# Kernel optimization log

Hardware: AMD Instinct MI355X
Metric: run time of the kernel (lower is better)

The kernel has to match this reference:

```python
import jax, jax.numpy as jnp
import numpy as np

ITERS = 3

def squash(s, axis):
    # v = (|s|^2 / (1 + |s|^2)) * s / |s|
    sn = jnp.sum(s * s, axis=axis, keepdims=True)
    return sn / (1.0 + sn) * s / jnp.sqrt(sn)

def setup_inputs() -> dict:
    key = jax.random.key(0)
    k1, k2 = jax.random.split(key)
    b, B, C, P2, f = 8, 144, 16, 16, 12
    u = jax.random.normal(k1, (b, B, C, P2, f, f), dtype=jnp.float32)
    a = jax.random.uniform(k2, (b, B, f, f), dtype=jnp.float32)
    return {"u": u, "a": a}

def reference(u, a):
    # u: (b, B, C, P2, f, f); a: (b, B, f, f)
    b, B, C, P2, f, _ = u.shape
    # r: (b, B, C, 1, f, f), initialized uniform over C scaled by activation
    r = jnp.broadcast_to(a[:, :, None, None, :, :] * (1.0 / C), (b, B, C, 1, f, f))
    v = None
    for i in range(ITERS):
        c = jax.nn.softmax(r, axis=2)                       # over C
        v = squash(jnp.sum(c * u, axis=1, keepdims=True), axis=3)  # (b,1,C,P2,f,f)
        if i != ITERS - 1:
            r = r + jnp.sum(u * v, axis=3, keepdims=True)   # agreement over psize
    a_out = jnp.sqrt(jnp.sum(v * v, axis=3, keepdims=True))  # (b,1,C,1,f,f)
    return (jnp.squeeze(v, axis=1), jnp.squeeze(a_out, axis=(1, 3)))
```

## Files before the change

### kernel.cpp

```cpp
#include <hip/hip_runtime.h>
#include <math.h>


#define NB 8
#define BDIM 144
#define CDIM 16
#define PDIM 16
#define SDIM 144
#define PT 16
#define BC 8
#define NPT (SDIM / PT)
#define NBC (BDIM / BC)
#define USTRIDE (CDIM * PDIM * SDIM)
#define VELEMS (NB * CDIM * PDIM * SDIM)
#define NGROUP (NB * NPT)

__global__ __launch_bounds__(256) void route_kernel(
    const float* __restrict__ u, const float* __restrict__ a,
    float* __restrict__ V, float* __restrict__ s,
    unsigned int* __restrict__ cnt,
    float* __restrict__ out_v, float* __restrict__ out_a, int iter) {
  __shared__ float Vt[CDIM][PDIM][PT + 1];
  __shared__ float ebuf[2][CDIM][PT + 1];
  __shared__ float atile[BC][PT];
  __shared__ int isLast;

  const int tid = threadIdx.x;
  const int pos = tid & 15;
  const int c = tid >> 4;
  const int chunk = blockIdx.x;
  const int y = blockIdx.y;
  const int b = blockIdx.z;
  const int posg = y * PT + pos;
  const int B0 = chunk * BC;

  const float* ubase =
      u + ((size_t)((b * BDIM + B0) * CDIM + c) * PDIM) * SDIM + posg;

  float sacc[PDIM];
#pragma unroll
  for (int p = 0; p < PDIM; ++p) sacc[p] = 0.f;

  if (iter == 0) {
#pragma unroll 2
    for (int j = 0; j < BC; ++j) {
      const float* ub = ubase + (size_t)j * USTRIDE;
#pragma unroll
      for (int p = 0; p < PDIM; ++p) sacc[p] += ub[p * SDIM];
    }
#pragma unroll
    for (int p = 0; p < PDIM; ++p) sacc[p] *= (1.0f / CDIM);
  } else {
    float uvbuf[2][PDIM];
#pragma unroll
    for (int p = 0; p < PDIM; ++p) uvbuf[0][p] = ubase[p * SDIM];

    {
      const int vb = ((b * CDIM + c) * PDIM) * SDIM + posg;
#pragma unroll
      for (int p = 0; p < PDIM; ++p) Vt[c][p][pos] = V[vb + p * SDIM];
      if (tid < BC * PT) {
        const int j = tid >> 4;
        atile[j][pos] =
            a[(b * BDIM + B0 + j) * SDIM + y * PT + pos] * (1.0f / CDIM);
      }
    }
    __syncthreads();

#pragma unroll
    for (int j = 0; j < BC; ++j) {
      float* uv = uvbuf[j & 1];
      float* uvn = uvbuf[(j + 1) & 1];
      if (j + 1 < BC) {
        const float* ub = ubase + (size_t)(j + 1) * USTRIDE;
#pragma unroll
        for (int p = 0; p < PDIM; ++p) uvn[p] = ub[p * SDIM];
      }
      float dot = 0.f;
#pragma unroll
      for (int p = 0; p < PDIM; ++p) dot += uv[p] * Vt[c][p][pos];
      const float e = __expf(atile[j][pos] + dot);
      ebuf[j & 1][c][pos] = e;
      asm volatile("s_waitcnt lgkmcnt(0)" ::: "memory");
      __builtin_amdgcn_s_barrier();
      float sum = 0.f;
#pragma unroll
      for (int c2 = 0; c2 < CDIM; ++c2) sum += ebuf[j & 1][c2][pos];
      const float w = e * __builtin_amdgcn_rcpf(sum);
#pragma unroll
      for (int p = 0; p < PDIM; ++p) sacc[p] += w * uv[p];
    }
  }

  const int base = ((b * CDIM + c) * PDIM) * SDIM + posg;
#pragma unroll
  for (int p = 0; p < PDIM; ++p) atomicAdd(&s[base + p * SDIM], sacc[p]);

  asm volatile("s_waitcnt vmcnt(0)" ::: "memory");
  __syncthreads();
  if (tid == 0) {
    const unsigned old = atomicAdd(&cnt[b * NPT + y], 1u);
    isLast = (old == (NBC - 1));
  }
  __syncthreads();
  if (!isLast) return;

  float sv[PDIM];
  float sn = 0.f;
#pragma unroll
  for (int p = 0; p < PDIM; ++p) {
    const float x = s[base + p * SDIM];
    sv[p] = x;
    sn += x * x;
  }
  const float scale = sn / (1.0f + sn) * rsqrtf(sn);

  if (iter == 0) {
#pragma unroll
    for (int p = 0; p < PDIM; ++p) V[base + p * SDIM] = sv[p] * scale;
  } else if (iter == 1) {
#pragma unroll
    for (int p = 0; p < PDIM; ++p) V[base + p * SDIM] += sv[p] * scale;
  } else {
    float vv = 0.f;
#pragma unroll
    for (int p = 0; p < PDIM; ++p) {
      const float v = sv[p] * scale;
      out_v[base + p * SDIM] = v;
      vv += v * v;
    }
    out_a[(b * CDIM + c) * SDIM + posg] = sqrtf(vv);
  }
}


extern "C" void kernel_launch(void* const* d_in, const int* in_sizes, int n_in,
                              void* d_out, int out_size, void* d_ws, size_t ws_size,
                              hipStream_t stream) {
  const float* u = (const float*)d_in[0];
  const float* a = (const float*)d_in[1];
  float* out_v = (float*)d_out;
  float* out_a = out_v + VELEMS;

  float* V = (float*)d_ws;
  float* s = V + VELEMS;
  unsigned int* cnt = (unsigned int*)(s + (size_t)3 * VELEMS);

  hipMemsetAsync(s, 0, (size_t)3 * VELEMS * sizeof(float) +
                           3 * NGROUP * sizeof(unsigned int), stream);

  const dim3 g(NBC, NPT, NB);
  for (int it = 0; it < 3; ++it)
    route_kernel<<<g, 256, 0, stream>>>(u, a, V, s + (size_t)it * VELEMS,
                                        cnt + it * NGROUP, out_v, out_a, it);
}
```

Baseline: 358.8 us.

## Replace atomics and LDS softmax with float4 wave-shuffle kernels plus separate reduce

Restructures routing into a per-chunk kernel of 64-thread blocks, where each lane handles one capsule and four spatial positions via float4 loads. The softmax over capsules uses wave shuffles instead of shared memory and barriers. Partial sums are written to a per-chunk buffer rather than accumulated with atomics, and a second kernel reduces them and applies squash. This removes atomics, the last-block counter and the memset, but adds six kernel launches and extra partial-buffer traffic, and the blocks are small enough that occupancy may suffer.

```diff
diff --git a/kernel.cpp b/kernel.cpp
--- a/kernel.cpp
+++ b/kernel.cpp
@@ -7,129 +7,160 @@
 #define CDIM 16
 #define PDIM 16
 #define SDIM 144
+#define NF4 (SDIM / 4)
 #define PT 16
 #define BC 8
 #define NPT (SDIM / PT)
 #define NBC (BDIM / BC)
-#define USTRIDE (CDIM * PDIM * SDIM)
+#define UF4STRIDE ((size_t)CDIM * PDIM * NF4)
 #define VELEMS (NB * CDIM * PDIM * SDIM)
-#define NGROUP (NB * NPT)
+#define VF4 (VELEMS / 4)
 
-__global__ __launch_bounds__(256) void route_kernel(
+static __device__ __forceinline__ float4 f4zero() {
+  return make_float4(0.f, 0.f, 0.f, 0.f);
+}
+static __device__ __forceinline__ float4 f4add(float4 a, float4 b) {
+  return make_float4(a.x + b.x, a.y + b.y, a.z + b.z, a.w + b.w);
+}
+static __device__ __forceinline__ float4 f4fma(float4 a, float4 b, float4 c) {
+  return make_float4(fmaf(a.x, b.x, c.x), fmaf(a.y, b.y, c.y),
+                     fmaf(a.z, b.z, c.z), fmaf(a.w, b.w, c.w));
+}
+static __device__ __forceinline__ float4 f4scale(float4 a, float s) {
+  return make_float4(a.x * s, a.y * s, a.z * s, a.w * s);
+}
+
+__global__ __launch_bounds__(64, 1) void route_f4(
     const float* __restrict__ u, const float* __restrict__ a,
-    float* __restrict__ V, float* __restrict__ s,
-    unsigned int* __restrict__ cnt,
-    float* __restrict__ out_v, float* __restrict__ out_a, int iter) {
-  __shared__ float Vt[CDIM][PDIM][PT + 1];
-  __shared__ float ebuf[2][CDIM][PT + 1];
-  __shared__ float atile[BC][PT];
-  __shared__ int isLast;
-
-  const int tid = threadIdx.x;
-  const int pos = tid & 15;
-  const int c = tid >> 4;
+    const float* __restrict__ V, float* __restrict__ part, int iter) {
+  const int lane = threadIdx.x;
+  const int c = lane >> 2;
+  const int posq = lane & 3;
   const int chunk = blockIdx.x;
   const int y = blockIdx.y;
   const int b = blockIdx.z;
-  const int posg = y * PT + pos;
+  const int f4 = y * 4 + posq;
   const int B0 = chunk * BC;
 
-  const float* ubase =
-      u + ((size_t)((b * BDIM + B0) * CDIM + c) * PDIM) * SDIM + posg;
+  const float4* ub = (const float4*)u +
+                     ((size_t)((b * BDIM + B0) * CDIM + c) * PDIM) * NF4 + f4;
 
-  float sacc[PDIM];
+  float4 sacc[PDIM];
 #pragma unroll
-  for (int p = 0; p < PDIM; ++p) sacc[p] = 0.f;
+  for (int p = 0; p < PDIM; ++p) sacc[p] = f4zero();
 
   if (iter == 0) {
 #pragma unroll 2
     for (int j = 0; j < BC; ++j) {
-      const float* ub = ubase + (size_t)j * USTRIDE;
+      const float4* up = ub + (size_t)j * UF4STRIDE;
 #pragma unroll
-      for (int p = 0; p < PDIM; ++p) sacc[p] += ub[p * SDIM];
+      for (int p = 0; p < PDIM; ++p) sacc[p] = f4add(sacc[p], up[p * NF4]);
     }
 #pragma unroll
-    for (int p = 0; p < PDIM; ++p) sacc[p] *= (1.0f / CDIM);
+    for (int p = 0; p < PDIM; ++p) sacc[p] = f4scale(sacc[p], 1.0f / CDIM);
   } else {
-    float uvbuf[2][PDIM];
+    float4 Vr[PDIM];
+    {
+      const float4* vb =
+          (const float4*)V + ((size_t)(b * CDIM + c) * PDIM) * NF4 + f4;
 #pragma unroll
-    for (int p = 0; p < PDIM; ++p) uvbuf[0][p] = ubase[p * SDIM];
-
-    {
-      const int vb = ((b * CDIM + c) * PDIM) * SDIM + posg;
+      for (int p = 0; p < PDIM; ++p) Vr[p] = vb[p * NF4];
+    }
+#pragma unroll 2
+    for (int j = 0; j < BC; ++j) {
+      const float4* up = ub + (size_t)j * UF4STRIDE;
+      float4 uu[PDIM];
 #pragma unroll
-      for (int p = 0; p < PDIM; ++p) Vt[c][p][pos] = V[vb + p * SDIM];
-      if (tid < BC * PT) {
-        const int j = tid >> 4;
-        atile[j][pos] =
-            a[(b * BDIM + B0 + j) * SDIM + y * PT + pos] * (1.0f / CDIM);
+      for (int p = 0; p < PDIM; ++p) uu[p] = up[p * NF4];
+      const float4 av =
+          ((const float4*)(a + (size_t)(b * BDIM + B0 + j) * SDIM))[f4];
+      float4 dot = f4scale(av, 1.0f / CDIM);
+#pragma unroll
+      for (int p = 0; p < PDIM; ++p) dot = f4fma(uu[p], Vr[p], dot);
+      float4 e;
+      e.x = __expf(dot.x); e.y = __expf(dot.y);
+      e.z = __expf(dot.z); e.w = __expf(dot.w);
+      float4 se = e;
+#pragma unroll
+      for (int m = 4; m <= 32; m <<= 1) {
+        se.x += __shfl_xor(se.x, m);
+        se.y += __shfl_xor(se.y, m);
+        se.z += __shfl_xor(se.z, m);
+        se.w += __shfl_xor(se.w, m);
       }
-    }
-    __syncthreads();
-
+      float4 w;
+      w.x = e.x * __builtin_amdgcn_rcpf(se.x);
+      w.y = e.y * __builtin_amdgcn_rcpf(se.y);
+      w.z = e.z * __builtin_amdgcn_rcpf(se.z);
+      w.w = e.w * __builtin_amdgcn_rcpf(se.w);
 #pragma unroll
-    for (int j = 0; j < BC; ++j) {
-      float* uv = uvbuf[j & 1];
-      float* uvn = uvbuf[(j + 1) & 1];
-      if (j + 1 < BC) {
-        const float* ub = ubase + (size_t)(j + 1) * USTRIDE;
-#pragma unroll
-        for (int p = 0; p < PDIM; ++p) uvn[p] = ub[p * SDIM];
-      }
-      float dot = 0.f;
-#pragma unroll
-      for (int p = 0; p < PDIM; ++p) dot += uv[p] * Vt[c][p][pos];
-      const float e = __expf(atile[j][pos] + dot);
-      ebuf[j & 1][c][pos] = e;
-      asm volatile("s_waitcnt lgkmcnt(0)" ::: "memory");
-      __builtin_amdgcn_s_barrier();
-      float sum = 0.f;
-#pragma unroll
-      for (int c2 = 0; c2 < CDIM; ++c2) sum += ebuf[j & 1][c2][pos];
-      const float w = e * __builtin_amdgcn_rcpf(sum);
-#pragma unroll
-      for (int p = 0; p < PDIM; ++p) sacc[p] += w * uv[p];
+      for (int p = 0; p < PDIM; ++p) sacc[p] = f4fma(w, uu[p], sacc[p]);
     }
   }
 
-  const int base = ((b * CDIM + c) * PDIM) * SDIM + posg;
+  float4* sp = (float4*)part + (size_t)chunk * VF4 +
+               ((size_t)(b * CDIM + c) * PDIM) * NF4 + f4;
 #pragma unroll
-  for (int p = 0; p < PDIM; ++p) atomicAdd(&s[base + p * SDIM], sacc[p]);
+  for (int p = 0; p < PDIM; ++p) sp[p * NF4] = sacc[p];
+}
 
-  asm volatile("s_waitcnt vmcnt(0)" ::: "memory");
-  __syncthreads();
-  if (tid == 0) {
-    const unsigned old = atomicAdd(&cnt[b * NPT + y], 1u);
-    isLast = (old == (NBC - 1));
+__global__ __launch_bounds__(64, 1) void reduce_f4(
+    const float* __restrict__ part, float* __restrict__ V,
+    float* __restrict__ out_v, float* __restrict__ out_a, int iter) {
+  const int lane = threadIdx.x;
+  const int c = lane >> 2;
+  const int posq = lane & 3;
+  const int y = blockIdx.x;
+  const int b = blockIdx.y;
+  const int f4 = y * 4 + posq;
+  const size_t base = ((size_t)(b * CDIM + c) * PDIM) * NF4 + f4;
+
+  float4 sv[PDIM];
+#pragma unroll
+  for (int p = 0; p < PDIM; ++p) sv[p] = f4zero();
+#pragma unroll 2
+  for (int k = 0; k < NBC; ++k) {
+    const float4* sp = (const float4*)part + (size_t)k * VF4 + base;
+#pragma unroll
+    for (int p = 0; p < PDIM; ++p) sv[p] = f4add(sv[p], sp[p * NF4]);
   }
-  __syncthreads();
-  if (!isLast) return;
 
-  float sv[PDIM];
-  float sn = 0.f;
+  float4 sn = f4zero();
 #pragma unroll
-  for (int p = 0; p < PDIM; ++p) {
-    const float x = s[base + p * SDIM];
-    sv[p] = x;
-    sn += x * x;
-  }
-  const float scale = sn / (1.0f + sn) * rsqrtf(sn);
+  for (int p = 0; p < PDIM; ++p) sn = f4fma(sv[p], sv[p], sn);
+  float4 sc;
+  sc.x = sn.x / (1.0f + sn.x) * rsqrtf(sn.x);
+  sc.y = sn.y / (1.0f + sn.y) * rsqrtf(sn.y);
+  sc.z = sn.z / (1.0f + sn.z) * rsqrtf(sn.z);
+  sc.w = sn.w / (1.0f + sn.w) * rsqrtf(sn.w);
 
+  float4* Vb = (float4*)V + base;
   if (iter == 0) {
 #pragma unroll
-    for (int p = 0; p < PDIM; ++p) V[base + p * SDIM] = sv[p] * scale;
+    for (int p = 0; p < PDIM; ++p) {
+      float4 v = sv[p];
+      Vb[p * NF4] = make_float4(v.x * sc.x, v.y * sc.y, v.z * sc.z, v.w * sc.w);
+    }
   } else if (iter == 1) {
 #pragma unroll
-    for (int p = 0; p < PDIM; ++p) V[base + p * SDIM] += sv[p] * scale;
+    for (int p = 0; p < PDIM; ++p) {
+      float4 v = sv[p];
+      float4 o = Vb[p * NF4];
+      Vb[p * NF4] = make_float4(fmaf(v.x, sc.x, o.x), fmaf(v.y, sc.y, o.y),
+                                fmaf(v.z, sc.z, o.z), fmaf(v.w, sc.w, o.w));
+    }
   } else {
-    float vv = 0.f;
+    float4 vv = f4zero();
+    float4* ov = (float4*)out_v + base;
 #pragma unroll
     for (int p = 0; p < PDIM; ++p) {
-      const float v = sv[p] * scale;
-      out_v[base + p * SDIM] = v;
-      vv += v * v;
+      float4 v = make_float4(sv[p].x * sc.x, sv[p].y * sc.y, sv[p].z * sc.z,
+                             sv[p].w * sc.w);
+      ov[p * NF4] = v;
+      vv = f4fma(v, v, vv);
     }
-    out_a[(b * CDIM + c) * SDIM + posg] = sqrtf(vv);
+    ((float4*)out_a)[(size_t)(b * CDIM + c) * NF4 + f4] =
+        make_float4(sqrtf(vv.x), sqrtf(vv.y), sqrtf(vv.z), sqrtf(vv.w));
   }
 }
 
@@ -143,14 +174,12 @@
   float* out_a = out_v + VELEMS;
 
   float* V = (float*)d_ws;
-  float* s = V + VELEMS;
-  unsigned int* cnt = (unsigned int*)(s + (size_t)3 * VELEMS);
+  float* part = V + VELEMS;
 
-  hipMemsetAsync(s, 0, (size_t)3 * VELEMS * sizeof(float) +
-                           3 * NGROUP * sizeof(unsigned int), stream);
-
-  const dim3 g(NBC, NPT, NB);
-  for (int it = 0; it < 3; ++it)
-    route_kernel<<<g, 256, 0, stream>>>(u, a, V, s + (size_t)it * VELEMS,
-                                        cnt + it * NGROUP, out_v, out_a, it);
+  const dim3 gR(NBC, NPT, NB);
+  const dim3 gQ(NPT, NB);
+  for (int it = 0; it < 3; ++it) {
+    route_f4<<<gR, 64, 0, stream>>>(u, a, V, part, it);
+    reduce_f4<<<gQ, 64, 0, stream>>>(part, V, out_v, out_a, it);
+  }
 }
```

Result: slower. 489.8 us (+36.5%).

## Stage u slabs in LDS with float4 loads and split spatial dim into thirds

Applied to the files above, without the earlier changes.

Each block now covers a third of the spatial positions (48 floats) instead of 16. Per capsule j it stages the u slab into padded LDS with coalesced float4 loads, and each of 192 active threads processes four positions with float4 math. V is held in registers, and a_out is computed in closed form as sn/(1+sn). The aims are wider, better-coalesced global loads and fewer, larger blocks. In exchange, 64 of 256 threads sit idle, each j step needs extra barriers, there is no prefetch overlap, and LDS use is large (about 50KB), which limits occupancy.

```diff
diff --git a/kernel.cpp b/kernel.cpp
--- a/kernel.cpp
+++ b/kernel.cpp
@@ -7,129 +7,173 @@
 #define CDIM 16
 #define PDIM 16
 #define SDIM 144
-#define PT 16
+#define NF4 (SDIM / 4)
 #define BC 8
-#define NPT (SDIM / PT)
 #define NBC (BDIM / BC)
-#define USTRIDE (CDIM * PDIM * SDIM)
+#define NTH 3
+#define Q 12
+#define NPAIR (CDIM * Q)
+#define SLABF4 (CDIM * PDIM * Q)
+#define PADC 194
 #define VELEMS (NB * CDIM * PDIM * SDIM)
-#define NGROUP (NB * NPT)
-
-__global__ __launch_bounds__(256) void route_kernel(
+#define NGROUP (NB * NTH)
+
+static __device__ __forceinline__ float4 f4zero() {
+  return make_float4(0.f, 0.f, 0.f, 0.f);
+}
+static __device__ __forceinline__ float4 f4fma(float4 a, float4 b, float4 c) {
+  return make_float4(fmaf(a.x, b.x, c.x), fmaf(a.y, b.y, c.y),
+                     fmaf(a.z, b.z, c.z), fmaf(a.w, b.w, c.w));
+}
+static __device__ __forceinline__ float4 f4scale(float4 a, float s) {
+  return make_float4(a.x * s, a.y * s, a.z * s, a.w * s);
+}
+
+__global__ __launch_bounds__(256) void route3(
     const float* __restrict__ u, const float* __restrict__ a,
-    float* __restrict__ V, float* __restrict__ s,
+    float* __restrict__ V, float* __restrict__ s_it,
     unsigned int* __restrict__ cnt,
     float* __restrict__ out_v, float* __restrict__ out_a, int iter) {
-  __shared__ float Vt[CDIM][PDIM][PT + 1];
-  __shared__ float ebuf[2][CDIM][PT + 1];
-  __shared__ float atile[BC][PT];
+  __shared__ float4 u_lds[CDIM * PADC];
+  __shared__ float4 e_lds[NPAIR];
   __shared__ int isLast;
 
   const int tid = threadIdx.x;
-  const int pos = tid & 15;
-  const int c = tid >> 4;
   const int chunk = blockIdx.x;
-  const int y = blockIdx.y;
+  const int third = blockIdx.y;
   const int b = blockIdx.z;
-  const int posg = y * PT + pos;
   const int B0 = chunk * BC;
-
-  const float* ubase =
-      u + ((size_t)((b * BDIM + B0) * CDIM + c) * PDIM) * SDIM + posg;
-
-  float sacc[PDIM];
-#pragma unroll
-  for (int p = 0; p < PDIM; ++p) sacc[p] = 0.f;
-
-  if (iter == 0) {
-#pragma unroll 2
-    for (int j = 0; j < BC; ++j) {
-      const float* ub = ubase + (size_t)j * USTRIDE;
-#pragma unroll
-      for (int p = 0; p < PDIM; ++p) sacc[p] += ub[p * SDIM];
-    }
-#pragma unroll
-    for (int p = 0; p < PDIM; ++p) sacc[p] *= (1.0f / CDIM);
-  } else {
-    float uvbuf[2][PDIM];
-#pragma unroll
-    for (int p = 0; p < PDIM; ++p) uvbuf[0][p] = ubase[p * SDIM];
-
-    {
-      const int vb = ((b * CDIM + c) * PDIM) * SDIM + posg;
-#pragma unroll
-      for (int p = 0; p < PDIM; ++p) Vt[c][p][pos] = V[vb + p * SDIM];
-      if (tid < BC * PT) {
-        const int j = tid >> 4;
-        atile[j][pos] =
-            a[(b * BDIM + B0 + j) * SDIM + y * PT + pos] * (1.0f / CDIM);
+  const int c = tid / Q;
+  const int q = tid - c * Q;
+  const bool act = (tid < NPAIR);
+
+  float4 Vr[PDIM];
+  if (iter != 0 && act) {
+    const float4* vb = (const float4*)V +
+                       ((size_t)(b * CDIM + c) * PDIM) * NF4 + third * Q + q;
+#pragma unroll
+    for (int p = 0; p < PDIM; ++p) Vr[p] = vb[p * NF4];
+  }
+
+  float4 sacc[PDIM];
+#pragma unroll
+  for (int p = 0; p < PDIM; ++p) sacc[p] = f4zero();
+
+  for (int j = 0; j < BC; ++j) {
+    const float4* gbase =
+        (const float4*)u + (size_t)(b * BDIM + B0 + j) * (CDIM * PDIM * NF4);
+#pragma unroll
+    for (int k = 0; k < SLABF4 / 256; ++k) {
+      const int fidx = k * 256 + tid;
+      const int c2 = fidx / (PDIM * Q);
+      const int rem = fidx - c2 * (PDIM * Q);
+      const int p2 = rem / Q;
+      const int q2 = rem - p2 * Q;
+      u_lds[c2 * PADC + p2 * Q + q2] =
+          gbase[(c2 * PDIM + p2) * NF4 + third * Q + q2];
+    }
+    __syncthreads();
+
+    float4 w4;
+    if (iter == 0) {
+      w4 = make_float4(1.0f / CDIM, 1.0f / CDIM, 1.0f / CDIM, 1.0f / CDIM);
+    } else {
+      if (act) {
+        float4 dot =
+            f4scale(((const float4*)a)[(size_t)(b * BDIM + B0 + j) * NF4 +
+                                       third * Q + q],
+                    1.0f / CDIM);
+#pragma unroll
+        for (int p = 0; p < PDIM; ++p)
+          dot = f4fma(u_lds[c * PADC + p * Q + q], Vr[p], dot);
+        float4 e;
+        e.x = __expf(dot.x); e.y = __expf(dot.y);
+        e.z = __expf(dot.z); e.w = __expf(dot.w);
+        e_lds[c * Q + q] = e;
       }
+      __syncthreads();
+      if (act) {
+        float4 se = f4zero();
+#pragma unroll
+        for (int c2 = 0; c2 < CDIM; ++c2) {
+          const float4 ev = e_lds[c2 * Q + q];
+          se.x += ev.x; se.y += ev.y; se.z += ev.z; se.w += ev.w;
+        }
+        const float4 e = e_lds[c * Q + q];
+        w4.x = e.x * __builtin_amdgcn_rcpf(se.x);
+        w4.y = e.y * __builtin_amdgcn_rcpf(se.y);
+        w4.z = e.z * __builtin_amdgcn_rcpf(se.z);
+        w4.w = e.w * __builtin_amdgcn_rcpf(se.w);
+      }
+    }
+    if (act) {
+#pragma unroll
+      for (int p = 0; p < PDIM; ++p)
+        sacc[p] = f4fma(w4, u_lds[c * PADC + p * Q + q], sacc[p]);
     }
     __syncthreads();
-
-#pragma unroll
-    for (int j = 0; j < BC; ++j) {
-      float* uv = uvbuf[j & 1];
-      float* uvn = uvbuf[(j + 1) & 1];
-      if (j + 1 < BC) {
-        const float* ub = ubase + (size_t)(j + 1) * USTRIDE;
-#pragma unroll
-        for (int p = 0; p < PDIM; ++p) uvn[p] = ub[p * SDIM];
-      }
-      float dot = 0.f;
-#pragma unroll
-      for (int p = 0; p < PDIM; ++p) dot += uv[p] * Vt[c][p][pos];
-      const float e = __expf(atile[j][pos] + dot);
-      ebuf[j & 1][c][pos] = e;
-      asm volatile("s_waitcnt lgkmcnt(0)" ::: "memory");
-      __builtin_amdgcn_s_barrier();
-      float sum = 0.f;
-#pragma unroll
-      for (int c2 = 0; c2 < CDIM; ++c2) sum += ebuf[j & 1][c2][pos];
-      const float w = e * __builtin_amdgcn_rcpf(sum);
-#pragma unroll
-      for (int p = 0; p < PDIM; ++p) sacc[p] += w * uv[p];
-    }
-  }
-
-  const int base = ((b * CDIM + c) * PDIM) * SDIM + posg;
-#pragma unroll
-  for (int p = 0; p < PDIM; ++p) atomicAdd(&s[base + p * SDIM], sacc[p]);
+  }
+
+  if (act) {
+    float* sp = s_it + ((size_t)(b * CDIM + c) * PDIM) * SDIM + third * 48 + q * 4;
+#pragma unroll
+    for (int p = 0; p < PDIM; ++p) {
+      atomicAdd(sp + p * SDIM + 0, sacc[p].x);
+      atomicAdd(sp + p * SDIM + 1, sacc[p].y);
+      atomicAdd(sp + p * SDIM + 2, sacc[p].z);
+      atomicAdd(sp + p * SDIM + 3, sacc[p].w);
+    }
+  }
 
   asm volatile("s_waitcnt vmcnt(0)" ::: "memory");
   __syncthreads();
   if (tid == 0) {
-    const unsigned old = atomicAdd(&cnt[b * NPT + y], 1u);
+    const unsigned old = atomicAdd(&cnt[b * NTH + third], 1u);
     isLast = (old == (NBC - 1));
   }
   __syncthreads();
   if (!isLast) return;
 
-  float sv[PDIM];
-  float sn = 0.f;
-#pragma unroll
-  for (int p = 0; p < PDIM; ++p) {
-    const float x = s[base + p * SDIM];
-    sv[p] = x;
-    sn += x * x;
-  }
-  const float scale = sn / (1.0f + sn) * rsqrtf(sn);
-
-  if (iter == 0) {
-#pragma unroll
-    for (int p = 0; p < PDIM; ++p) V[base + p * SDIM] = sv[p] * scale;
-  } else if (iter == 1) {
-#pragma unroll
-    for (int p = 0; p < PDIM; ++p) V[base + p * SDIM] += sv[p] * scale;
-  } else {
-    float vv = 0.f;
+  if (act) {
+    const size_t idx =
+        ((size_t)(b * CDIM + c) * PDIM) * NF4 + third * Q + q;
+    float4 sv[PDIM];
+    float4 sn = f4zero();
 #pragma unroll
     for (int p = 0; p < PDIM; ++p) {
-      const float v = sv[p] * scale;
-      out_v[base + p * SDIM] = v;
-      vv += v * v;
-    }
-    out_a[(b * CDIM + c) * SDIM + posg] = sqrtf(vv);
+      sv[p] = ((const float4*)s_it)[idx + p * NF4];
+      sn = f4fma(sv[p], sv[p], sn);
+    }
+    float4 sc;
+    sc.x = sn.x / (1.0f + sn.x) * rsqrtf(sn.x);
+    sc.y = sn.y / (1.0f + sn.y) * rsqrtf(sn.y);
+    sc.z = sn.z / (1.0f + sn.z) * rsqrtf(sn.z);
+    sc.w = sn.w / (1.0f + sn.w) * rsqrtf(sn.w);
+
+    if (iter == 0) {
+      float4* Vb = (float4*)V + idx;
+#pragma unroll
+      for (int p = 0; p < PDIM; ++p)
+        Vb[p * NF4] = make_float4(sv[p].x * sc.x, sv[p].y * sc.y,
+                                  sv[p].z * sc.z, sv[p].w * sc.w);
+    } else if (iter == 1) {
+      float4* Vb = (float4*)V + idx;
+#pragma unroll
+      for (int p = 0; p < PDIM; ++p)
+        Vb[p * NF4] = make_float4(fmaf(sv[p].x, sc.x, Vr[p].x),
+                                  fmaf(sv[p].y, sc.y, Vr[p].y),
+                                  fmaf(sv[p].z, sc.z, Vr[p].z),
+                                  fmaf(sv[p].w, sc.w, Vr[p].w));
+    } else {
+      float4* ov = (float4*)out_v + idx;
+#pragma unroll
+      for (int p = 0; p < PDIM; ++p)
+        ov[p * NF4] = make_float4(sv[p].x * sc.x, sv[p].y * sc.y,
+                                  sv[p].z * sc.z, sv[p].w * sc.w);
+      ((float4*)out_a)[(size_t)(b * CDIM + c) * NF4 + third * Q + q] =
+          make_float4(sn.x / (1.0f + sn.x), sn.y / (1.0f + sn.y),
+                      sn.z / (1.0f + sn.z), sn.w / (1.0f + sn.w));
+    }
   }
 }
 
@@ -149,8 +193,8 @@
   hipMemsetAsync(s, 0, (size_t)3 * VELEMS * sizeof(float) +
                            3 * NGROUP * sizeof(unsigned int), stream);
 
-  const dim3 g(NBC, NPT, NB);
+  const dim3 g(NBC, NTH, NB);
   for (int it = 0; it < 3; ++it)
-    route_kernel<<<g, 256, 0, stream>>>(u, a, V, s + (size_t)it * VELEMS,
-                                        cnt + it * NGROUP, out_v, out_a, it);
-}
+    route3<<<g, 256, 0, stream>>>(u, a, V, s + (size_t)it * VELEMS,
+                                  cnt + it * NGROUP, out_v, out_a, it);
+}
```

Measured after the change: 490.4 us. 1.37x slower.
